# Kernel optimization log

Hardware: AMD Instinct MI355X
Metric: run time of the kernel (lower is better)

Reference implementation:

```python
import jax, jax.numpy as jnp
import numpy as np

N = 8192        # total nodes (64 graphs x 128 nodes)
B = 64          # graphs in batch
E0 = 32768      # explicit edges (self-loops added in forward)
IN = 32         # input node feats
H = [64, 64]    # hidden feats per NNConv layer
BOND = 5        # bond (edge) feature dim, hard-coded in source


def setup_inputs() -> dict:
    key = jax.random.key(0)
    ks = jax.random.split(key, 16)
    s = 0.1
    node_feats = jax.random.normal(ks[0], (N, IN), jnp.float32)
    edge_feats = jax.random.normal(ks[1], (E0, BOND), jnp.float32)
    src = jax.random.randint(ks[2], (E0,), 0, N)
    dst = jax.random.randint(ks[3], (E0,), 0, N)
    graph_ids = jnp.repeat(jnp.arange(B), N // B)  # contiguous batched graphs
    timestep = jax.random.randint(ks[4], (B, 1), 0, 1000).astype(jnp.float32)
    # NNConv layer 1: edge MLP Linear(BOND, IN*H0) + output bias
    edge_W1 = jax.random.normal(ks[5], (BOND, IN * H[0]), jnp.float32) * s
    edge_b1 = jax.random.normal(ks[6], (IN * H[0],), jnp.float32) * s
    bias1 = jax.random.normal(ks[7], (H[0],), jnp.float32) * s
    # NNConv layer 2: edge MLP Linear(BOND, H0*H1) + output bias
    edge_W2 = jax.random.normal(ks[8], (BOND, H[0] * H[1]), jnp.float32) * s
    edge_b2 = jax.random.normal(ks[9], (H[0] * H[1],), jnp.float32) * s
    bias2 = jax.random.normal(ks[10], (H[1],), jnp.float32) * s
    # WeightAndSum pooling: Linear(H1, 1) + sigmoid
    ws_W = jax.random.normal(ks[11], (H[1], 1), jnp.float32) * s
    ws_b = jax.random.normal(ks[12], (1,), jnp.float32) * s
    return {
        "node_feats": node_feats, "edge_feats": edge_feats,
        "src": src, "dst": dst, "graph_ids": graph_ids, "timestep": timestep,
        "edge_W1": edge_W1, "edge_b1": edge_b1, "bias1": bias1,
        "edge_W2": edge_W2, "edge_b2": edge_b2, "bias2": bias2,
        "ws_W": ws_W, "ws_b": ws_b,
    }


def _nnconv(h, ef, src, dst, edge_W, edge_b, bias, din, dout):
    # edge MLP -> per-edge weight matrix [E, din, dout]
    W = (ef @ edge_W + edge_b).reshape(-1, din, dout)
    # gather source feats, per-edge matmul, scatter-sum to destinations
    m = jnp.einsum('ei,eio->eo', h[src], W)
    agg = jax.ops.segment_sum(m, dst, num_segments=N)
    return agg + bias


def reference(node_feats, edge_feats, src, dst, graph_ids, timestep,
              edge_W1, edge_b1, bias1, edge_W2, edge_b2, bias2, ws_W, ws_b):
    # add self-loops with zero edge features (forward does dgl.add_self_loop)
    loop = jnp.arange(N)
    src_a = jnp.concatenate([src, loop])
    dst_a = jnp.concatenate([dst, loop])
    ef = jnp.concatenate([edge_feats, jnp.zeros((N, BOND), edge_feats.dtype)])

    h = jax.nn.relu(_nnconv(node_feats, ef, src_a, dst_a, edge_W1, edge_b1, bias1, IN, H[0]))
    h = jax.nn.relu(_nnconv(h, ef, src_a, dst_a, edge_W2, edge_b2, bias2, H[0], H[1]))

    # WeightAndSum pooling + max pooling per graph
    w = jax.nn.sigmoid(h @ ws_W + ws_b)                     # [N,1]
    g_sum = jax.ops.segment_sum(h * w, graph_ids, num_segments=B)
    g_max = jax.ops.segment_max(h, graph_ids, num_segments=B)
    graph_feats = jnp.concatenate([g_sum, g_max], axis=1)    # [B, 2*H1]

    # sinusoidal timestep conditioning (channels = 2*H1 = 128)
    C = 2 * H[-1]
    inv_freq = 1.0 / (10000.0 ** (jnp.arange(0, C, 2).astype(jnp.float32) / C))
    arg = timestep * inv_freq                                # [B, C//2]
    pos_enc = jnp.concatenate([jnp.sin(arg), jnp.cos(arg)], axis=-1)
    graph_feats = graph_feats + pos_enc

    return jnp.tanh(jax.nn.relu(graph_feats))
```

## Files before the change

kernel.cpp:

```cpp
#include <hip/hip_runtime.h>
#include <math.h>

#define N_NODES 8192
#define NEDGE   32768
#define BGRAPH  64

template <int DIN>
__global__ __launch_bounds__(384) void transform_kernel(
    const float* __restrict__ h_in,
    const float* __restrict__ edge_W,
    const float* __restrict__ edge_b,
    const float* __restrict__ bias,
    float* __restrict__ TS,
    float* __restrict__ agg,
    int relu_in) {
  __shared__ float hTile[16][DIN];
  const int n0 = blockIdx.x * 16;

  for (int idx = threadIdx.x; idx < 16 * DIN; idx += 384) {
    float v = h_in[(size_t)n0 * DIN + idx];
    if (relu_in) v = fmaxf(v, 0.0f);
    hTile[idx / DIN][idx % DIN] = v;
  }
  __syncthreads();

  const int j = threadIdx.x;
  const int o = j & 63;
  const bool isS = (j >= 320);
  const float* wsrc = isS ? (edge_b + o)
                          : (edge_W + (size_t)(j >> 6) * (DIN * 64) + o);
  float wcol[DIN];
#pragma unroll
  for (int i = 0; i < DIN; ++i) wcol[i] = wsrc[(size_t)i * 64];
  const float bo = bias[o];

  for (int n = 0; n < 16; ++n) {
    float acc = 0.0f;
#pragma unroll
    for (int i = 0; i < DIN; ++i) acc = fmaf(hTile[n][i], wcol[i], acc);
    TS[(size_t)(n0 + n) * 384 + j] = acc;
    if (isS) agg[(size_t)(n0 + n) * 64 + o] = acc + bo;
  }
}

__global__ __launch_bounds__(256) void edge_kernel(
    const float* __restrict__ ef,
    const int* __restrict__ src,
    const int* __restrict__ dst,
    const float* __restrict__ TS,
    float* __restrict__ agg) {
  const int e = (blockIdx.x * 256 + threadIdx.x) >> 6;
  const int o = threadIdx.x & 63;
  if (e >= NEDGE) return;

  const int s = src[e];
  const int d = dst[e];
  const float c0 = ef[(size_t)e * 5 + 0];
  const float c1 = ef[(size_t)e * 5 + 1];
  const float c2 = ef[(size_t)e * 5 + 2];
  const float c3 = ef[(size_t)e * 5 + 3];
  const float c4 = ef[(size_t)e * 5 + 4];

  const float* row = TS + (size_t)s * 384;
  float m = row[320 + o];
  m = fmaf(c0, row[o], m);
  m = fmaf(c1, row[64 + o], m);
  m = fmaf(c2, row[128 + o], m);
  m = fmaf(c3, row[192 + o], m);
  m = fmaf(c4, row[256 + o], m);

  atomicAdd(&agg[(size_t)d * 64 + o], m);
}

__global__ __launch_bounds__(256) void pool_kernel(
    const float* __restrict__ agg2,
    const float* __restrict__ ws_W,
    const float* __restrict__ ws_b,
    const float* __restrict__ timestep,
    float* __restrict__ out) {
  __shared__ float tile[128][65];
  __shared__ float wn[128];
  __shared__ float partS[4][64];
  __shared__ float partM[4][64];
  __shared__ float wsw[64];

  const int g = blockIdx.x;
  const int t = threadIdx.x;

  const float* base = agg2 + (size_t)g * 128 * 64;
  for (int idx = t; idx < 128 * 64; idx += 256) {
    tile[idx >> 6][idx & 63] = fmaxf(base[idx], 0.0f);
  }
  if (t < 64) wsw[t] = ws_W[t];
  __syncthreads();

  if (t < 128) {
    float acc = ws_b[0];
    for (int o = 0; o < 64; ++o) acc = fmaf(tile[t][o], wsw[o], acc);
    wn[t] = 1.0f / (1.0f + expf(-acc));
  }
  __syncthreads();

  const int o = t & 63;
  const int q = t >> 6;
  float s = 0.0f, mx = 0.0f;
  for (int n = q * 32; n < q * 32 + 32; ++n) {
    const float v = tile[n][o];
    s = fmaf(v, wn[n], s);
    mx = fmaxf(mx, v);
  }
  partS[q][o] = s;
  partM[q][o] = mx;
  __syncthreads();

  if (t < 128) {
    const int c = t;
    const int oo = c & 63;
    float val;
    if (c < 64) {
      val = partS[0][oo] + partS[1][oo] + partS[2][oo] + partS[3][oo];
    } else {
      val = fmaxf(fmaxf(partM[0][oo], partM[1][oo]),
                  fmaxf(partM[2][oo], partM[3][oo]));
    }
    const float invf = exp2f(-(float)oo * (13.287712379549449f / 64.0f));
    const float ang = timestep[g] * invf;
    const float pe = (c < 64) ? sinf(ang) : cosf(ang);
    out[(size_t)g * 128 + c] = tanhf(fmaxf(val + pe, 0.0f));
  }
}

extern "C" void kernel_launch(void* const* d_in, const int* in_sizes, int n_in,
                              void* d_out, int out_size, void* d_ws, size_t ws_size,
                              hipStream_t stream) {
  const float* node_feats = (const float*)d_in[0];
  const float* edge_feats = (const float*)d_in[1];
  const int*   src        = (const int*)d_in[2];
  const int*   dst        = (const int*)d_in[3];
  const float* timestep   = (const float*)d_in[5];
  const float* edge_W1    = (const float*)d_in[6];
  const float* edge_b1    = (const float*)d_in[7];
  const float* bias1      = (const float*)d_in[8];
  const float* edge_W2    = (const float*)d_in[9];
  const float* edge_b2    = (const float*)d_in[10];
  const float* bias2      = (const float*)d_in[11];
  const float* ws_W       = (const float*)d_in[12];
  const float* ws_b       = (const float*)d_in[13];
  float* out = (float*)d_out;

  float* TS   = (float*)d_ws;
  float* agg1 = TS + (size_t)N_NODES * 384;
  float* agg2 = agg1 + (size_t)N_NODES * 64;

  transform_kernel<32><<<N_NODES / 16, 384, 0, stream>>>(
      node_feats, edge_W1, edge_b1, bias1, TS, agg1, 0);
  edge_kernel<<<NEDGE / 4, 256, 0, stream>>>(edge_feats, src, dst, TS, agg1);
  transform_kernel<64><<<N_NODES / 16, 384, 0, stream>>>(
      agg1, edge_W2, edge_b2, bias2, TS, agg2, 1);
  edge_kernel<<<NEDGE / 4, 256, 0, stream>>>(edge_feats, src, dst, TS, agg2);
  pool_kernel<<<BGRAPH, 256, 0, stream>>>(agg2, ws_W, ws_b, timestep, out);
}
```

Before: 139.1 us.

## Fuse all five stages into one cooperative persistent kernel with grid syncs

Replaces the five separate launches (two transforms, two edge scatters, pooling) with one cooperative kernel of 256 blocks. The blocks step through the phases separated by grid.sync, and each block handles a fixed slice of nodes and edges. This is meant to remove per-launch overhead and the gaps between the small kernels. In exchange, 256 blocks give less parallelism per phase than the earlier grids, and every grid barrier has its own cost.

```diff
diff --git a/kernel.cpp b/kernel.cpp
--- a/kernel.cpp
+++ b/kernel.cpp
@@ -1,102 +1,110 @@
 #include <hip/hip_runtime.h>
+#include <hip/hip_cooperative_groups.h>
 #include <math.h>
 
-#define N_NODES 8192
-#define NEDGE   32768
-#define BGRAPH  64
+namespace cg = cooperative_groups;
+
+#define NN   8192
+#define NE   32768
+#define NB   256
+#define NT   384
+#define NPB  (NN / NB)
+#define EPB  (NE / NB)
+
+
+__shared__ float smem[9280];
 
 template <int DIN>
-__global__ __launch_bounds__(384) void transform_kernel(
+__device__ __forceinline__ void transform_phase(
     const float* __restrict__ h_in,
-    const float* __restrict__ edge_W,
-    const float* __restrict__ edge_b,
+    const float* __restrict__ eW,
+    const float* __restrict__ eb,
     const float* __restrict__ bias,
     float* __restrict__ TS,
     float* __restrict__ agg,
-    int relu_in) {
-  __shared__ float hTile[16][DIN];
-  const int n0 = blockIdx.x * 16;
-
-  for (int idx = threadIdx.x; idx < 16 * DIN; idx += 384) {
+    int bid, int tid, bool relu_in) {
+  float* tile = smem;
+  const int n0 = bid * NPB;
+  for (int idx = tid; idx < NPB * DIN; idx += NT) {
     float v = h_in[(size_t)n0 * DIN + idx];
     if (relu_in) v = fmaxf(v, 0.0f);
-    hTile[idx / DIN][idx % DIN] = v;
+    tile[idx] = v;
   }
   __syncthreads();
 
-  const int j = threadIdx.x;
+  const int j = tid;
   const int o = j & 63;
   const bool isS = (j >= 320);
-  const float* wsrc = isS ? (edge_b + o)
-                          : (edge_W + (size_t)(j >> 6) * (DIN * 64) + o);
+  const float* wsrc = isS ? (eb + o) : (eW + (size_t)(j >> 6) * (DIN * 64) + o);
   float wcol[DIN];
 #pragma unroll
   for (int i = 0; i < DIN; ++i) wcol[i] = wsrc[(size_t)i * 64];
   const float bo = bias[o];
 
-  for (int n = 0; n < 16; ++n) {
+  for (int n = 0; n < NPB; ++n) {
     float acc = 0.0f;
 #pragma unroll
-    for (int i = 0; i < DIN; ++i) acc = fmaf(hTile[n][i], wcol[i], acc);
+    for (int i = 0; i < DIN; ++i) acc = fmaf(tile[n * DIN + i], wcol[i], acc);
     TS[(size_t)(n0 + n) * 384 + j] = acc;
     if (isS) agg[(size_t)(n0 + n) * 64 + o] = acc + bo;
   }
+  __syncthreads();
 }
 
-__global__ __launch_bounds__(256) void edge_kernel(
+__device__ __forceinline__ void edge_phase(
     const float* __restrict__ ef,
     const int* __restrict__ src,
     const int* __restrict__ dst,
     const float* __restrict__ TS,
-    float* __restrict__ agg) {
-  const int e = (blockIdx.x * 256 + threadIdx.x) >> 6;
-  const int o = threadIdx.x & 63;
-  if (e >= NEDGE) return;
-
-  const int s = src[e];
-  const int d = dst[e];
-  const float c0 = ef[(size_t)e * 5 + 0];
-  const float c1 = ef[(size_t)e * 5 + 1];
-  const float c2 = ef[(size_t)e * 5 + 2];
-  const float c3 = ef[(size_t)e * 5 + 3];
-  const float c4 = ef[(size_t)e * 5 + 4];
-
-  const float* row = TS + (size_t)s * 384;
-  float m = row[320 + o];
-  m = fmaf(c0, row[o], m);
-  m = fmaf(c1, row[64 + o], m);
-  m = fmaf(c2, row[128 + o], m);
-  m = fmaf(c3, row[192 + o], m);
-  m = fmaf(c4, row[256 + o], m);
-
-  atomicAdd(&agg[(size_t)d * 64 + o], m);
+    float* __restrict__ agg,
+    int bid, int tid) {
+  const int wave = tid >> 6;
+  const int o = tid & 63;
+  const int e0 = bid * EPB;
+  const int e1 = e0 + EPB;
+#pragma unroll 2
+  for (int e = e0 + wave; e < e1; e += 6) {
+    const int s = src[e];
+    const int d = dst[e];
+    const float c0 = ef[(size_t)e * 5 + 0];
+    const float c1 = ef[(size_t)e * 5 + 1];
+    const float c2 = ef[(size_t)e * 5 + 2];
+    const float c3 = ef[(size_t)e * 5 + 3];
+    const float c4 = ef[(size_t)e * 5 + 4];
+    const float* row = TS + (size_t)s * 384;
+    float m = row[320 + o];
+    m = fmaf(c0, row[o], m);
+    m = fmaf(c1, row[64 + o], m);
+    m = fmaf(c2, row[128 + o], m);
+    m = fmaf(c3, row[192 + o], m);
+    m = fmaf(c4, row[256 + o], m);
+    atomicAdd(&agg[(size_t)d * 64 + o], m);
+  }
 }
 
-__global__ __launch_bounds__(256) void pool_kernel(
+__device__ __forceinline__ void pool_phase(
     const float* __restrict__ agg2,
     const float* __restrict__ ws_W,
     const float* __restrict__ ws_b,
     const float* __restrict__ timestep,
-    float* __restrict__ out) {
-  __shared__ float tile[128][65];
-  __shared__ float wn[128];
-  __shared__ float partS[4][64];
-  __shared__ float partM[4][64];
-  __shared__ float wsw[64];
-
-  const int g = blockIdx.x;
-  const int t = threadIdx.x;
+    float* __restrict__ out,
+    int g, int t) {
+  float* tile  = smem;
+  float* wn    = smem + 128 * 65;
+  float* partS = wn + 128;
+  float* partM = partS + 6 * 64;
+  float* wsw   = partM + 6 * 64;
 
   const float* base = agg2 + (size_t)g * 128 * 64;
-  for (int idx = t; idx < 128 * 64; idx += 256) {
-    tile[idx >> 6][idx & 63] = fmaxf(base[idx], 0.0f);
+  for (int idx = t; idx < 128 * 64; idx += NT) {
+    tile[(idx >> 6) * 65 + (idx & 63)] = fmaxf(base[idx], 0.0f);
   }
   if (t < 64) wsw[t] = ws_W[t];
   __syncthreads();
 
   if (t < 128) {
     float acc = ws_b[0];
-    for (int o = 0; o < 64; ++o) acc = fmaf(tile[t][o], wsw[o], acc);
+    for (int o = 0; o < 64; ++o) acc = fmaf(tile[t * 65 + o], wsw[o], acc);
     wn[t] = 1.0f / (1.0f + expf(-acc));
   }
   __syncthreads();
@@ -104,30 +112,56 @@
   const int o = t & 63;
   const int q = t >> 6;
   float s = 0.0f, mx = 0.0f;
-  for (int n = q * 32; n < q * 32 + 32; ++n) {
-    const float v = tile[n][o];
+  for (int n = q; n < 128; n += 6) {
+    const float v = tile[n * 65 + o];
     s = fmaf(v, wn[n], s);
     mx = fmaxf(mx, v);
   }
-  partS[q][o] = s;
-  partM[q][o] = mx;
+  partS[q * 64 + o] = s;
+  partM[q * 64 + o] = mx;
   __syncthreads();
 
   if (t < 128) {
-    const int c = t;
-    const int oo = c & 63;
+    const int oo = t & 63;
     float val;
-    if (c < 64) {
-      val = partS[0][oo] + partS[1][oo] + partS[2][oo] + partS[3][oo];
+    if (t < 64) {
+      val = 0.0f;
+      for (int k = 0; k < 6; ++k) val += partS[k * 64 + oo];
     } else {
-      val = fmaxf(fmaxf(partM[0][oo], partM[1][oo]),
-                  fmaxf(partM[2][oo], partM[3][oo]));
+      val = 0.0f;
+      for (int k = 0; k < 6; ++k) val = fmaxf(val, partM[k * 64 + oo]);
     }
     const float invf = exp2f(-(float)oo * (13.287712379549449f / 64.0f));
     const float ang = timestep[g] * invf;
-    const float pe = (c < 64) ? sinf(ang) : cosf(ang);
-    out[(size_t)g * 128 + c] = tanhf(fmaxf(val + pe, 0.0f));
+    const float pe = (t < 64) ? sinf(ang) : cosf(ang);
+    out[(size_t)g * 128 + t] = tanhf(fmaxf(val + pe, 0.0f));
   }
+}
+
+__global__ __launch_bounds__(NT) void fused_gcn(
+    const float* __restrict__ node_feats, const float* __restrict__ edge_feats,
+    const int* __restrict__ src, const int* __restrict__ dst,
+    const float* __restrict__ timestep,
+    const float* __restrict__ edge_W1, const float* __restrict__ edge_b1,
+    const float* __restrict__ bias1,
+    const float* __restrict__ edge_W2, const float* __restrict__ edge_b2,
+    const float* __restrict__ bias2,
+    const float* __restrict__ ws_W, const float* __restrict__ ws_b,
+    float* __restrict__ TS, float* __restrict__ agg1, float* __restrict__ agg2,
+    float* __restrict__ out) {
+  const int bid = blockIdx.x;
+  const int tid = threadIdx.x;
+  cg::grid_group grid = cg::this_grid();
+
+  transform_phase<32>(node_feats, edge_W1, edge_b1, bias1, TS, agg1, bid, tid, false);
+  grid.sync();
+  edge_phase(edge_feats, src, dst, TS, agg1, bid, tid);
+  grid.sync();
+  transform_phase<64>(agg1, edge_W2, edge_b2, bias2, TS, agg2, bid, tid, true);
+  grid.sync();
+  edge_phase(edge_feats, src, dst, TS, agg2, bid, tid);
+  grid.sync();
+  if (bid < 64) pool_phase(agg2, ws_W, ws_b, timestep, out, bid, tid);
 }
 
 extern "C" void kernel_launch(void* const* d_in, const int* in_sizes, int n_in,
@@ -149,14 +183,16 @@
   float* out = (float*)d_out;
 
   float* TS   = (float*)d_ws;
-  float* agg1 = TS + (size_t)N_NODES * 384;
-  float* agg2 = agg1 + (size_t)N_NODES * 64;
+  float* agg1 = TS + (size_t)NN * 384;
+  float* agg2 = agg1 + (size_t)NN * 64;
 
-  transform_kernel<32><<<N_NODES / 16, 384, 0, stream>>>(
-      node_feats, edge_W1, edge_b1, bias1, TS, agg1, 0);
-  edge_kernel<<<NEDGE / 4, 256, 0, stream>>>(edge_feats, src, dst, TS, agg1);
-  transform_kernel<64><<<N_NODES / 16, 384, 0, stream>>>(
-      agg1, edge_W2, edge_b2, bias2, TS, agg2, 1);
-  edge_kernel<<<NEDGE / 4, 256, 0, stream>>>(edge_feats, src, dst, TS, agg2);
-  pool_kernel<<<BGRAPH, 256, 0, stream>>>(agg2, ws_W, ws_b, timestep, out);
+  void* args[] = {
+      (void*)&node_feats, (void*)&edge_feats, (void*)&src, (void*)&dst,
+      (void*)&timestep,
+      (void*)&edge_W1, (void*)&edge_b1, (void*)&bias1,
+      (void*)&edge_W2, (void*)&edge_b2, (void*)&bias2,
+      (void*)&ws_W, (void*)&ws_b,
+      (void*)&TS, (void*)&agg1, (void*)&agg2, (void*)&out};
+  hipLaunchCooperativeKernel((const void*)fused_gcn, dim3(NB), dim3(NT),
+                             args, 0, stream);
 }
```

Result: slower. 275.6 us (+98.2%).
